# Optimization experiments

Hardware: AMD Instinct MI355X
Metric: run time of the kernel (lower is better)

Reference implementation:

```python
import jax, jax.numpy as jnp
import numpy as np

B, L, D, H = 2, 2048, 1024, 16


def setup_inputs() -> dict:
    key = jax.random.key(0)
    ks = jax.random.split(key, 6)
    return {
        "x": jax.random.normal(ks[0], (B, L, D), dtype=jnp.float32),
        "w_qkv": jax.random.normal(ks[1], (3 * D, D), dtype=jnp.float32) * (D ** -0.5),
        "b_qkv": jax.random.normal(ks[2], (3 * D,), dtype=jnp.float32) * 0.02,
        "w_out": jax.random.normal(ks[3], (D, D), dtype=jnp.float32) * (D ** -0.5),
        "b_out": jax.random.normal(ks[4], (D,), dtype=jnp.float32) * 0.02,
        "lam": jnp.float32(0.5),
        "heads": H,
    }


def reference(x, w_qkv, b_qkv, w_out, b_out, lam, heads):
    b, l, d = x.shape
    dh = d // heads
    scale = d ** -0.5  # NOTE: module scales by d_model**-0.5, not head_dim**-0.5

    qkv = x @ w_qkv.T + b_qkv                      # [B, L, 3D]
    qkv = qkv.reshape(b, l, 3, heads, dh)
    qkv = jnp.transpose(qkv, (2, 0, 3, 1, 4))      # [3, B, H, L, dh]
    q, k, v = qkv[0], qkv[1], qkv[2]

    k_prev = jnp.roll(k, shift=1, axis=2)          # roll along sequence dim

    s_cur = jnp.einsum("bhqd,bhkd->bhqk", q, k) * scale
    s_prev = jnp.einsum("bhqd,bhkd->bhqk", q, k_prev) * scale

    a1 = jax.nn.softmax(s_cur, axis=-1)
    a2 = jax.nn.softmax(s_prev, axis=-1)
    diff = lam * (a1 - a2)                         # dropout = identity (eval)

    o = jnp.einsum("bhqk,bhkd->bhqd", diff, v)     # [B, H, L, dh]
    o = jnp.transpose(o, (0, 2, 1, 3)).reshape(b, l, d)
    return o @ w_out.T + b_out
```

## Files before the change

### kernel.cpp

```cpp
#include <hip/hip_runtime.h>
#include <hip/hip_bf16.h>
#include <stdint.h>


typedef __attribute__((ext_vector_type(8))) short s16x8;
typedef __attribute__((ext_vector_type(4))) short s16x4;
typedef __attribute__((ext_vector_type(4))) float f32x4;

__device__ __forceinline__ float bf2f(unsigned short u) {
    union { unsigned int i; float f; } x; x.i = ((unsigned int)u) << 16; return x.f;
}
__device__ __forceinline__ unsigned short f2bf(float f) {
    union { float f; unsigned int i; } x; x.f = f;
    unsigned int r = x.i + 0x7FFFu + ((x.i >> 16) & 1u);
    return (unsigned short)(r >> 16);
}

__device__ __forceinline__ f32x4 mfma16(s16x4 a, s16x4 b, f32x4 c) {
#if __has_builtin(__builtin_amdgcn_mfma_f32_16x16x16bf16_1k)
    return __builtin_amdgcn_mfma_f32_16x16x16bf16_1k(a, b, c, 0, 0, 0);
#else
    f32x4 d;
    asm volatile("v_mfma_f32_16x16x16_bf16 %0, %1, %2, %3\n\ts_nop 7\n\ts_nop 3"
                 : "=v"(d) : "v"(a), "v"(b), "v"(c));
    return d;
#endif
}

__device__ __forceinline__ void gload16(const void* g, void* l) {
    auto gp = reinterpret_cast<const __attribute__((address_space(1))) unsigned int*>(
        reinterpret_cast<uintptr_t>(g));
    auto lp = reinterpret_cast<__attribute__((address_space(3))) unsigned int*>(
        reinterpret_cast<uintptr_t>(l));
    __builtin_amdgcn_global_load_lds(gp, lp, 16, 0, 0);
}

__global__ __launch_bounds__(256) void cvt_all(
    const float* __restrict__ x, const float* __restrict__ wq,
    const float* __restrict__ wo,
    unsigned short* __restrict__ xb, unsigned short* __restrict__ wqb,
    unsigned short* __restrict__ wob)
{
    int i4 = blockIdx.x * 256 + threadIdx.x;
    const float* src; unsigned short* dst; int off;
    if (i4 < 1048576)            { src = x;  dst = xb;  off = i4; }
    else if (i4 < 1048576 + 786432) { src = wq; dst = wqb; off = i4 - 1048576; }
    else                         { src = wo; dst = wob; off = i4 - 1835008; }
    float4 v = ((const float4*)src)[off];
    ushort4 u;
    u.x = f2bf(v.x); u.y = f2bf(v.y); u.z = f2bf(v.z); u.w = f2bf(v.w);
    ((ushort4*)dst)[off] = u;
}

__global__ __launch_bounds__(256) void vd_transpose(
    const unsigned short* __restrict__ qkvb, unsigned short* __restrict__ vdt)
{
    __shared__ unsigned short T[64][72];
    const int tid = threadIdx.x;
    const int j0 = blockIdx.x * 64;
    const int bh = blockIdx.y, b = bh >> 4, h = bh & 15;
    const unsigned short* vb = qkvb + (size_t)b * 2048 * 3072 + 2048 + h * 64;

    int r = tid >> 2, cq = tid & 3;
    int j = j0 + r, jn = (j + 1) & 2047;
    const unsigned short* p0 = vb + (size_t)j  * 3072 + cq * 16;
    const unsigned short* p1 = vb + (size_t)jn * 3072 + cq * 16;
    s16x8 a0 = *(const s16x8*)p0, a1 = *(const s16x8*)(p0 + 8);
    s16x8 b0 = *(const s16x8*)p1, b1 = *(const s16x8*)(p1 + 8);
#pragma unroll
    for (int u = 0; u < 8; ++u)
        T[cq * 16 + u][r] = f2bf(bf2f((unsigned short)a0[u]) - bf2f((unsigned short)b0[u]));
#pragma unroll
    for (int u = 0; u < 8; ++u)
        T[cq * 16 + 8 + u][r] = f2bf(bf2f((unsigned short)a1[u]) - bf2f((unsigned short)b1[u]));
    __syncthreads();

    int row = tid >> 2, sc = tid & 3;
    s16x8 o0 = *(const s16x8*)&T[row][sc * 16];
    s16x8 o1 = *(const s16x8*)&T[row][sc * 16 + 8];
    unsigned short* dst = vdt + ((size_t)bh * 64 + row) * 2048 + j0 + sc * 16;
    *(s16x8*)dst = o0;
    *(s16x8*)(dst + 8) = o1;
}

template <int OUT_BF16, int BN>
__global__ __launch_bounds__(256) void gemm_nt_mfma(
    const unsigned short* __restrict__ A,
    const unsigned short* __restrict__ Bm,
    const float* __restrict__ bias,
    void* __restrict__ C,
    int M, int N, int K, int nscale, float smul)
{
    constexpr int NT = BN / 32;
    __shared__ unsigned short As[2][128][32];
    __shared__ unsigned short Bs[2][BN][32];

    const int tid = threadIdx.x;
    const int wave = tid >> 6, lane = tid & 63;
    const int quad = lane >> 4, ln = lane & 15;
    const int wm = (wave >> 1) * 64, wn = (wave & 1) * (NT * 16);
    const int m0 = blockIdx.y * 128, n0 = blockIdx.x * BN;
    const int rA = wave * 16 + (lane >> 2);
    const int gsl = lane & 3;

    f32x4 acc[4][NT];
#pragma unroll
    for (int mt = 0; mt < 4; ++mt)
#pragma unroll
        for (int nt = 0; nt < NT; ++nt) acc[mt][nt] = f32x4{0.f, 0.f, 0.f, 0.f};

    auto stage = [&](int p, int k0) {
#pragma unroll
        for (int q = 0; q < 2; ++q) {
            int row = q * 64 + rA;
            int kg = gsl ^ ((row >> 1) & 3);
            gload16(A + (size_t)(m0 + row) * K + k0 + kg * 8,
                    &As[p][q * 64 + wave * 16][0]);
            if (q * 64 < BN)
                gload16(Bm + (size_t)(n0 + row) * K + k0 + kg * 8,
                        &Bs[p][q * 64 + wave * 16][0]);
        }
    };

    stage(0, 0);
    __syncthreads();
    int p = 0;
    for (int k0 = 0; k0 < K; k0 += 32) {
        if (k0 + 32 < K) stage(p ^ 1, k0 + 32);
        s16x8 af[4], bfr[NT];
#pragma unroll
        for (int mt = 0; mt < 4; ++mt) {
            int rr = wm + mt * 16 + ln;
            af[mt] = *(const s16x8*)&As[p][rr][((quad ^ ((rr >> 1) & 3)) & 3) * 8];
        }
#pragma unroll
        for (int nt = 0; nt < NT; ++nt) {
            int rr = wn + nt * 16 + ln;
            bfr[nt] = *(const s16x8*)&Bs[p][rr][((quad ^ ((rr >> 1) & 3)) & 3) * 8];
        }
#pragma unroll
        for (int mt = 0; mt < 4; ++mt)
#pragma unroll
            for (int nt = 0; nt < NT; ++nt)
                acc[mt][nt] = __builtin_amdgcn_mfma_f32_16x16x32_bf16(
                    af[mt], bfr[nt], acc[mt][nt], 0, 0, 0);
        __syncthreads();
        p ^= 1;
    }

    float bb[NT];
#pragma unroll
    for (int nt = 0; nt < NT; ++nt) bb[nt] = bias[n0 + wn + nt * 16 + ln];
#pragma unroll
    for (int mt = 0; mt < 4; ++mt)
#pragma unroll
        for (int nt = 0; nt < NT; ++nt) {
            int col = n0 + wn + nt * 16 + ln;
            float sc = (col < nscale) ? smul : 1.f;
#pragma unroll
            for (int rg = 0; rg < 4; ++rg) {
                int row = m0 + wm + mt * 16 + quad * 4 + rg;
                float v = (acc[mt][nt][rg] + bb[nt]) * sc;
                if (OUT_BF16)
                    ((unsigned short*)C)[(size_t)row * N + col] = f2bf(v);
                else
                    ((float*)C)[(size_t)row * N + col] = v;
            }
        }
}

__global__ __launch_bounds__(256) void diff_attn_v5(
    const unsigned short* __restrict__ qkv,
    const unsigned short* __restrict__ vdt,
    const float* __restrict__ lam_p,
    unsigned short* __restrict__ o_ws)
{
    constexpr int L = 2048, TD = 3072;

    __shared__ unsigned short Ks[2][64][64];
    __shared__ unsigned short Vs[2][64][64];

    const int tid = threadIdx.x;
    const int wave = tid >> 6, lane = tid & 63;
    const int quad = lane >> 4, ln = lane & 15;
    const int bh = blockIdx.y, b = bh >> 4, h = bh & 15;
    const int q0 = blockIdx.x * 128;
    const size_t seqbase = (size_t)b * L;
    const unsigned short* base = qkv + seqbase * TD + h * 64;
    const unsigned short* kb = base + 1024;
    const unsigned short* vbase = vdt + (size_t)bh * 64 * 2048;

    const int lsl = lane >> 3;
    const int cgl = (lane & 7) ^ lsl;

    s16x8 qf[2][2];
#pragma unroll
    for (int s = 0; s < 2; ++s) {
        const unsigned short* qrow =
            base + (size_t)(q0 + wave * 32 + s * 16 + ln) * TD;
        qf[s][0] = *(const s16x8*)(qrow + quad * 8);
        qf[s][1] = *(const s16x8*)(qrow + 32 + quad * 8);
    }

    auto stage = [&](int p, int j0) {
        const unsigned short* k0p = kb + (size_t)(j0 + wave * 16 + lsl) * TD + cgl * 8;
        gload16(k0p,                  &Ks[p][wave * 16][0]);
        gload16(k0p + (size_t)8 * TD, &Ks[p][wave * 16 + 8][0]);
        const unsigned short* v0p = vbase + (size_t)(wave * 16 + lsl) * 2048 + j0 + cgl * 8;
        gload16(v0p,            &Vs[p][wave * 16][0]);
        gload16(v0p + 8 * 2048, &Vs[p][wave * 16 + 8][0]);
    };

    f32x4 Ot[2][4];
    f32x4 lacc[2];
#pragma unroll
    for (int s = 0; s < 2; ++s) {
        lacc[s] = f32x4{0.f, 0.f, 0.f, 0.f};
#pragma unroll
        for (int mt = 0; mt < 4; ++mt) Ot[s][mt] = f32x4{0.f, 0.f, 0.f, 0.f};
    }

    const s16x4 ones = {(short)0x3F80, (short)0x3F80, (short)0x3F80, (short)0x3F80};
    const int kx0 = (quad ^ (ln & 7)) << 3;
    const int kx1 = ((quad + 4) ^ (ln & 7)) << 3;

    stage(0, 0);
    __syncthreads();
    int p = 0;
    for (int kt = 0; kt < 32; ++kt) {
        if (kt + 1 < 32) stage(p ^ 1, (kt + 1) * 64);

        f32x4 ST[2][4];
#pragma unroll
        for (int t = 0; t < 4; ++t) {
            s16x8 k0 = *(const s16x8*)&Ks[p][t * 16 + ln][kx0];
            s16x8 k1 = *(const s16x8*)&Ks[p][t * 16 + ln][kx1];
#pragma unroll
            for (int s = 0; s < 2; ++s) {
                f32x4 z = f32x4{0.f, 0.f, 0.f, 0.f};
                z = __builtin_amdgcn_mfma_f32_16x16x32_bf16(k0, qf[s][0], z, 0, 0, 0);
                z = __builtin_amdgcn_mfma_f32_16x16x32_bf16(k1, qf[s][1], z, 0, 0, 0);
                ST[s][t] = z;
            }
        }

        s16x4 pf[2][4];
#pragma unroll
        for (int s = 0; s < 2; ++s)
#pragma unroll
            for (int t = 0; t < 4; ++t) {
                unsigned int b0 = __builtin_bit_cast(unsigned int,
                    __builtin_amdgcn_exp2f(ST[s][t][0]));
                unsigned int b1 = __builtin_bit_cast(unsigned int,
                    __builtin_amdgcn_exp2f(ST[s][t][1]));
                unsigned int b2 = __builtin_bit_cast(unsigned int,
                    __builtin_amdgcn_exp2f(ST[s][t][2]));
                unsigned int b3 = __builtin_bit_cast(unsigned int,
                    __builtin_amdgcn_exp2f(ST[s][t][3]));
                unsigned int lo = (b0 >> 16) | (b1 & 0xFFFF0000u);
                unsigned int hi = (b2 >> 16) | (b3 & 0xFFFF0000u);
                uint2 pk = make_uint2(lo, hi);
                pf[s][t] = __builtin_bit_cast(s16x4, pk);
            }

#pragma unroll
        for (int s = 0; s < 2; ++s)
#pragma unroll
            for (int t = 0; t < 4; ++t)
                lacc[s] = mfma16(ones, pf[s][t], lacc[s]);

#pragma unroll
        for (int t = 0; t < 4; ++t) {
#pragma unroll
            for (int mt = 0; mt < 4; ++mt) {
                int chunk = (2 * t + (quad >> 1)) ^ (ln & 7);
                s16x4 vf = *(const s16x4*)&Vs[p][mt * 16 + ln][chunk * 8 + (quad & 1) * 4];
#pragma unroll
                for (int s = 0; s < 2; ++s)
                    Ot[s][mt] = mfma16(vf, pf[s][t], Ot[s][mt]);
            }
        }
        __syncthreads();
        p ^= 1;
    }

    const float lam = lam_p[0];
#pragma unroll
    for (int s = 0; s < 2; ++s) {
        float inv = lam / lacc[s][0];
        int row = q0 + wave * 32 + s * 16 + ln;
        unsigned short* orow = o_ws + (seqbase + row) * 1024 + h * 64 + quad * 4;
#pragma unroll
        for (int mt = 0; mt < 4; ++mt) {
            ushort4 u;
            u.x = f2bf(Ot[s][mt][0] * inv);
            u.y = f2bf(Ot[s][mt][1] * inv);
            u.z = f2bf(Ot[s][mt][2] * inv);
            u.w = f2bf(Ot[s][mt][3] * inv);
            *(ushort4*)(orow + mt * 16) = u;
        }
    }
}

extern "C" void kernel_launch(void* const* d_in, const int* in_sizes, int n_in,
                              void* d_out, int out_size, void* d_ws, size_t ws_size,
                              hipStream_t stream) {
    const float* x     = (const float*)d_in[0];
    const float* w_qkv = (const float*)d_in[1];
    const float* b_qkv = (const float*)d_in[2];
    const float* w_out = (const float*)d_in[3];
    const float* b_out = (const float*)d_in[4];
    const float* lam   = (const float*)d_in[5];
    float* out = (float*)d_out;

    unsigned short* xb   = (unsigned short*)d_ws;
    unsigned short* wqb  = xb   + (size_t)4096 * 1024;
    unsigned short* wob  = wqb  + (size_t)3072 * 1024;
    unsigned short* qkvb = wob  + (size_t)1024 * 1024;
    unsigned short* ob   = qkvb + (size_t)4096 * 3072;
    unsigned short* vdt  = ob   + (size_t)4096 * 1024;

    cvt_all<<<8192, 256, 0, stream>>>(x, w_qkv, w_out, xb, wqb, wob);

    gemm_nt_mfma<1, 128><<<dim3(24, 32), 256, 0, stream>>>(
        xb, wqb, b_qkv, qkvb, 4096, 3072, 1024, 1024, 0.045084222f);

    vd_transpose<<<dim3(32, 32), 256, 0, stream>>>(qkvb, vdt);

    diff_attn_v5<<<dim3(16, 32), 256, 0, stream>>>(qkvb, vdt, lam, ob);

    gemm_nt_mfma<0, 64><<<dim3(16, 32), 256, 0, stream>>>(
        ob, wob, b_out, out, 4096, 1024, 1024, 0, 1.f);
}
```

Measured before the change: 198.4 us.

## Use 16x16x32 MFMA for PV via permlane swaps and halve query tile

The attention kernel now converts exp'd scores into operands for the 16x16x32 bf16 MFMA using v_permlane32/16_swap, replacing the 16x16x16 MFMAs for both the row-sum and PV products. It also reads V with 8-element vector loads matching the K swizzle. Each block now handles 64 query rows instead of 128, one 16-row slice per wave, and the grid doubles. Fewer, wider MFMAs and more blocks should raise throughput and occupancy, but K/V tiles are reused across half as many queries per block, doubling their global and LDS traffic.

```diff
diff --git a/kernel.cpp b/kernel.cpp
--- a/kernel.cpp
+++ b/kernel.cpp
@@ -4,7 +4,6 @@
 
 
 typedef __attribute__((ext_vector_type(8))) short s16x8;
-typedef __attribute__((ext_vector_type(4))) short s16x4;
 typedef __attribute__((ext_vector_type(4))) float f32x4;
 
 __device__ __forceinline__ float bf2f(unsigned short u) {
@@ -14,17 +13,6 @@
     union { float f; unsigned int i; } x; x.f = f;
     unsigned int r = x.i + 0x7FFFu + ((x.i >> 16) & 1u);
     return (unsigned short)(r >> 16);
-}
-
-__device__ __forceinline__ f32x4 mfma16(s16x4 a, s16x4 b, f32x4 c) {
-#if __has_builtin(__builtin_amdgcn_mfma_f32_16x16x16bf16_1k)
-    return __builtin_amdgcn_mfma_f32_16x16x16bf16_1k(a, b, c, 0, 0, 0);
-#else
-    f32x4 d;
-    asm volatile("v_mfma_f32_16x16x16_bf16 %0, %1, %2, %3\n\ts_nop 7\n\ts_nop 3"
-                 : "=v"(d) : "v"(a), "v"(b), "v"(c));
-    return d;
-#endif
 }
 
 __device__ __forceinline__ void gload16(const void* g, void* l) {
@@ -169,7 +157,7 @@
         }
 }
 
-__global__ __launch_bounds__(256) void diff_attn_v5(
+__global__ __launch_bounds__(256) void diff_attn_v6(
     const unsigned short* __restrict__ qkv,
     const unsigned short* __restrict__ vdt,
     const float* __restrict__ lam_p,
@@ -184,7 +172,7 @@
     const int wave = tid >> 6, lane = tid & 63;
     const int quad = lane >> 4, ln = lane & 15;
     const int bh = blockIdx.y, b = bh >> 4, h = bh & 15;
-    const int q0 = blockIdx.x * 128;
+    const int q0 = blockIdx.x * 64;
     const size_t seqbase = (size_t)b * L;
     const unsigned short* base = qkv + seqbase * TD + h * 64;
     const unsigned short* kb = base + 1024;
@@ -193,13 +181,11 @@
     const int lsl = lane >> 3;
     const int cgl = (lane & 7) ^ lsl;
 
-    s16x8 qf[2][2];
-#pragma unroll
-    for (int s = 0; s < 2; ++s) {
-        const unsigned short* qrow =
-            base + (size_t)(q0 + wave * 32 + s * 16 + ln) * TD;
-        qf[s][0] = *(const s16x8*)(qrow + quad * 8);
-        qf[s][1] = *(const s16x8*)(qrow + 32 + quad * 8);
+    s16x8 qf0, qf1;
+    {
+        const unsigned short* qrow = base + (size_t)(q0 + wave * 16 + ln) * TD;
+        qf0 = *(const s16x8*)(qrow + quad * 8);
+        qf1 = *(const s16x8*)(qrow + 32 + quad * 8);
     }
 
     auto stage = [&](int p, int j0) {
@@ -211,16 +197,14 @@
         gload16(v0p + 8 * 2048, &Vs[p][wave * 16 + 8][0]);
     };
 
-    f32x4 Ot[2][4];
-    f32x4 lacc[2];
-#pragma unroll
-    for (int s = 0; s < 2; ++s) {
-        lacc[s] = f32x4{0.f, 0.f, 0.f, 0.f};
-#pragma unroll
-        for (int mt = 0; mt < 4; ++mt) Ot[s][mt] = f32x4{0.f, 0.f, 0.f, 0.f};
-    }
-
-    const s16x4 ones = {(short)0x3F80, (short)0x3F80, (short)0x3F80, (short)0x3F80};
+    f32x4 Ot[4];
+    f32x4 lacc;
+    lacc = f32x4{0.f, 0.f, 0.f, 0.f};
+#pragma unroll
+    for (int mt = 0; mt < 4; ++mt) Ot[mt] = f32x4{0.f, 0.f, 0.f, 0.f};
+
+    const s16x8 ones8 = {(short)0x3F80, (short)0x3F80, (short)0x3F80, (short)0x3F80,
+                         (short)0x3F80, (short)0x3F80, (short)0x3F80, (short)0x3F80};
     const int kx0 = (quad ^ (ln & 7)) << 3;
     const int kx1 = ((quad + 4) ^ (ln & 7)) << 3;
 
@@ -230,54 +214,51 @@
     for (int kt = 0; kt < 32; ++kt) {
         if (kt + 1 < 32) stage(p ^ 1, (kt + 1) * 64);
 
-        f32x4 ST[2][4];
+        f32x4 ST[4];
 #pragma unroll
         for (int t = 0; t < 4; ++t) {
             s16x8 k0 = *(const s16x8*)&Ks[p][t * 16 + ln][kx0];
             s16x8 k1 = *(const s16x8*)&Ks[p][t * 16 + ln][kx1];
-#pragma unroll
-            for (int s = 0; s < 2; ++s) {
-                f32x4 z = f32x4{0.f, 0.f, 0.f, 0.f};
-                z = __builtin_amdgcn_mfma_f32_16x16x32_bf16(k0, qf[s][0], z, 0, 0, 0);
-                z = __builtin_amdgcn_mfma_f32_16x16x32_bf16(k1, qf[s][1], z, 0, 0, 0);
-                ST[s][t] = z;
-            }
-        }
-
-        s16x4 pf[2][4];
-#pragma unroll
-        for (int s = 0; s < 2; ++s)
-#pragma unroll
-            for (int t = 0; t < 4; ++t) {
-                unsigned int b0 = __builtin_bit_cast(unsigned int,
-                    __builtin_amdgcn_exp2f(ST[s][t][0]));
-                unsigned int b1 = __builtin_bit_cast(unsigned int,
-                    __builtin_amdgcn_exp2f(ST[s][t][1]));
-                unsigned int b2 = __builtin_bit_cast(unsigned int,
-                    __builtin_amdgcn_exp2f(ST[s][t][2]));
-                unsigned int b3 = __builtin_bit_cast(unsigned int,
-                    __builtin_amdgcn_exp2f(ST[s][t][3]));
-                unsigned int lo = (b0 >> 16) | (b1 & 0xFFFF0000u);
-                unsigned int hi = (b2 >> 16) | (b3 & 0xFFFF0000u);
-                uint2 pk = make_uint2(lo, hi);
-                pf[s][t] = __builtin_bit_cast(s16x4, pk);
-            }
-
-#pragma unroll
-        for (int s = 0; s < 2; ++s)
-#pragma unroll
-            for (int t = 0; t < 4; ++t)
-                lacc[s] = mfma16(ones, pf[s][t], lacc[s]);
-
+            f32x4 z = f32x4{0.f, 0.f, 0.f, 0.f};
+            z = __builtin_amdgcn_mfma_f32_16x16x32_bf16(k0, qf0, z, 0, 0, 0);
+            z = __builtin_amdgcn_mfma_f32_16x16x32_bf16(k1, qf1, z, 0, 0, 0);
+            ST[t] = z;
+        }
+
+        uint2 pk[4];
 #pragma unroll
         for (int t = 0; t < 4; ++t) {
+            unsigned int e0 = __builtin_bit_cast(unsigned int, __builtin_amdgcn_exp2f(ST[t][0]));
+            unsigned int e1 = __builtin_bit_cast(unsigned int, __builtin_amdgcn_exp2f(ST[t][1]));
+            unsigned int e2 = __builtin_bit_cast(unsigned int, __builtin_amdgcn_exp2f(ST[t][2]));
+            unsigned int e3 = __builtin_bit_cast(unsigned int, __builtin_amdgcn_exp2f(ST[t][3]));
+            pk[t].x = (e0 >> 16) | (e1 & 0xFFFF0000u);
+            pk[t].y = (e2 >> 16) | (e3 & 0xFFFF0000u);
+        }
+
+        s16x8 pfr[2];
+#pragma unroll
+        for (int bb = 0; bb < 2; ++bb) {
+            unsigned int a0 = pk[2 * bb].x, b0 = pk[2 * bb + 1].x;
+            unsigned int a1 = pk[2 * bb].y, b1 = pk[2 * bb + 1].y;
+            asm volatile("v_permlane32_swap_b32 %0, %1" : "+v"(a0), "+v"(b0));
+            asm volatile("v_permlane16_swap_b32 %0, %1" : "+v"(a0), "+v"(b0));
+            asm volatile("v_permlane32_swap_b32 %0, %1" : "+v"(a1), "+v"(b1));
+            asm volatile("v_permlane16_swap_b32 %0, %1" : "+v"(a1), "+v"(b1));
+            uint4 fr = make_uint4(a0, a1, b0, b1);
+            pfr[bb] = __builtin_bit_cast(s16x8, fr);
+        }
+
+        lacc = __builtin_amdgcn_mfma_f32_16x16x32_bf16(ones8, pfr[0], lacc, 0, 0, 0);
+        lacc = __builtin_amdgcn_mfma_f32_16x16x32_bf16(ones8, pfr[1], lacc, 0, 0, 0);
+
+#pragma unroll
+        for (int bb = 0; bb < 2; ++bb) {
+            const int kx = bb ? kx1 : kx0;
 #pragma unroll
             for (int mt = 0; mt < 4; ++mt) {
-                int chunk = (2 * t + (quad >> 1)) ^ (ln & 7);
-                s16x4 vf = *(const s16x4*)&Vs[p][mt * 16 + ln][chunk * 8 + (quad & 1) * 4];
-#pragma unroll
-                for (int s = 0; s < 2; ++s)
-                    Ot[s][mt] = mfma16(vf, pf[s][t], Ot[s][mt]);
+                s16x8 vf = *(const s16x8*)&Vs[p][mt * 16 + ln][kx];
+                Ot[mt] = __builtin_amdgcn_mfma_f32_16x16x32_bf16(vf, pfr[bb], Ot[mt], 0, 0, 0);
             }
         }
         __syncthreads();
@@ -285,18 +266,17 @@
     }
 
     const float lam = lam_p[0];
-#pragma unroll
-    for (int s = 0; s < 2; ++s) {
-        float inv = lam / lacc[s][0];
-        int row = q0 + wave * 32 + s * 16 + ln;
+    {
+        float inv = lam / lacc[0];
+        int row = q0 + wave * 16 + ln;
         unsigned short* orow = o_ws + (seqbase + row) * 1024 + h * 64 + quad * 4;
 #pragma unroll
         for (int mt = 0; mt < 4; ++mt) {
             ushort4 u;
-            u.x = f2bf(Ot[s][mt][0] * inv);
-            u.y = f2bf(Ot[s][mt][1] * inv);
-            u.z = f2bf(Ot[s][mt][2] * inv);
-            u.w = f2bf(Ot[s][mt][3] * inv);
+            u.x = f2bf(Ot[mt][0] * inv);
+            u.y = f2bf(Ot[mt][1] * inv);
+            u.z = f2bf(Ot[mt][2] * inv);
+            u.w = f2bf(Ot[mt][3] * inv);
             *(ushort4*)(orow + mt * 16) = u;
         }
     }
@@ -327,7 +307,7 @@
 
     vd_transpose<<<dim3(32, 32), 256, 0, stream>>>(qkvb, vdt);
 
-    diff_attn_v5<<<dim3(16, 32), 256, 0, stream>>>(qkvb, vdt, lam, ob);
+    diff_attn_v6<<<dim3(32, 32), 256, 0, stream>>>(qkvb, vdt, lam, ob);
 
     gemm_nt_mfma<0, 64><<<dim3(16, 32), 256, 0, stream>>>(
         ob, wob, b_out, out, 4096, 1024, 1024, 0, 1.f);
```

Measured after the change: 199.7 us. No clear change (+0.7%).

## Use 16x16x32 MFMA for PV via permlane swaps; shrink attention blocks to two waves

Applied to the files above, without the earlier changes.

The PV product and row-sum accumulation move from 16x16x16 bf16 MFMAs to 16x16x32 MFMAs. The exp'd probability fragments are rearranged across lanes with v_permlane32/16_swap so they match the wider K-operand layout, and V is read as 8-element chunks reusing the K swizzle offsets. This halves the MFMA instruction count for that stage. The attention kernel also drops to 128 threads covering 64 query rows per block, doubling the grid, with each wave now staging 32 K/V rows. The cost is extra cross-lane swap instructions and fewer waves per block to hide load latency.

```diff
diff --git a/kernel.cpp b/kernel.cpp
--- a/kernel.cpp
+++ b/kernel.cpp
@@ -4,7 +4,6 @@
 
 
 typedef __attribute__((ext_vector_type(8))) short s16x8;
-typedef __attribute__((ext_vector_type(4))) short s16x4;
 typedef __attribute__((ext_vector_type(4))) float f32x4;
 
 __device__ __forceinline__ float bf2f(unsigned short u) {
@@ -14,17 +13,6 @@
     union { float f; unsigned int i; } x; x.f = f;
     unsigned int r = x.i + 0x7FFFu + ((x.i >> 16) & 1u);
     return (unsigned short)(r >> 16);
-}
-
-__device__ __forceinline__ f32x4 mfma16(s16x4 a, s16x4 b, f32x4 c) {
-#if __has_builtin(__builtin_amdgcn_mfma_f32_16x16x16bf16_1k)
-    return __builtin_amdgcn_mfma_f32_16x16x16bf16_1k(a, b, c, 0, 0, 0);
-#else
-    f32x4 d;
-    asm volatile("v_mfma_f32_16x16x16_bf16 %0, %1, %2, %3\n\ts_nop 7\n\ts_nop 3"
-                 : "=v"(d) : "v"(a), "v"(b), "v"(c));
-    return d;
-#endif
 }
 
 __device__ __forceinline__ void gload16(const void* g, void* l) {
@@ -169,7 +157,7 @@
         }
 }
 
-__global__ __launch_bounds__(256) void diff_attn_v5(
+__global__ __launch_bounds__(128) void diff_attn_v7(
     const unsigned short* __restrict__ qkv,
     const unsigned short* __restrict__ vdt,
     const float* __restrict__ lam_p,
@@ -184,7 +172,7 @@
     const int wave = tid >> 6, lane = tid & 63;
     const int quad = lane >> 4, ln = lane & 15;
     const int bh = blockIdx.y, b = bh >> 4, h = bh & 15;
-    const int q0 = blockIdx.x * 128;
+    const int q0 = blockIdx.x * 64;
     const size_t seqbase = (size_t)b * L;
     const unsigned short* base = qkv + seqbase * TD + h * 64;
     const unsigned short* kb = base + 1024;
@@ -203,12 +191,15 @@
     }
 
     auto stage = [&](int p, int j0) {
-        const unsigned short* k0p = kb + (size_t)(j0 + wave * 16 + lsl) * TD + cgl * 8;
-        gload16(k0p,                  &Ks[p][wave * 16][0]);
-        gload16(k0p + (size_t)8 * TD, &Ks[p][wave * 16 + 8][0]);
-        const unsigned short* v0p = vbase + (size_t)(wave * 16 + lsl) * 2048 + j0 + cgl * 8;
-        gload16(v0p,            &Vs[p][wave * 16][0]);
-        gload16(v0p + 8 * 2048, &Vs[p][wave * 16 + 8][0]);
+        const unsigned short* k0p = kb + (size_t)(j0 + wave * 32 + lsl) * TD + cgl * 8;
+#pragma unroll
+        for (int rr = 0; rr < 4; ++rr)
+            gload16(k0p + (size_t)(8 * rr) * TD, &Ks[p][wave * 32 + 8 * rr][0]);
+        const unsigned short* v0p =
+            vbase + (size_t)(wave * 32 + lsl) * 2048 + j0 + cgl * 8;
+#pragma unroll
+        for (int rr = 0; rr < 4; ++rr)
+            gload16(v0p + 8 * rr * 2048, &Vs[p][wave * 32 + 8 * rr][0]);
     };
 
     f32x4 Ot[2][4];
@@ -220,7 +211,8 @@
         for (int mt = 0; mt < 4; ++mt) Ot[s][mt] = f32x4{0.f, 0.f, 0.f, 0.f};
     }
 
-    const s16x4 ones = {(short)0x3F80, (short)0x3F80, (short)0x3F80, (short)0x3F80};
+    const s16x8 ones8 = {(short)0x3F80, (short)0x3F80, (short)0x3F80, (short)0x3F80,
+                         (short)0x3F80, (short)0x3F80, (short)0x3F80, (short)0x3F80};
     const int kx0 = (quad ^ (ln & 7)) << 3;
     const int kx1 = ((quad + 4) ^ (ln & 7)) << 3;
 
@@ -244,40 +236,44 @@
             }
         }
 
-        s16x4 pf[2][4];
-#pragma unroll
-        for (int s = 0; s < 2; ++s)
+        s16x8 pfr[2][2];
+#pragma unroll
+        for (int s = 0; s < 2; ++s) {
+            uint2 pk[4];
 #pragma unroll
             for (int t = 0; t < 4; ++t) {
-                unsigned int b0 = __builtin_bit_cast(unsigned int,
-                    __builtin_amdgcn_exp2f(ST[s][t][0]));
-                unsigned int b1 = __builtin_bit_cast(unsigned int,
-                    __builtin_amdgcn_exp2f(ST[s][t][1]));
-                unsigned int b2 = __builtin_bit_cast(unsigned int,
-                    __builtin_amdgcn_exp2f(ST[s][t][2]));
-                unsigned int b3 = __builtin_bit_cast(unsigned int,
-                    __builtin_amdgcn_exp2f(ST[s][t][3]));
-                unsigned int lo = (b0 >> 16) | (b1 & 0xFFFF0000u);
-                unsigned int hi = (b2 >> 16) | (b3 & 0xFFFF0000u);
-                uint2 pk = make_uint2(lo, hi);
-                pf[s][t] = __builtin_bit_cast(s16x4, pk);
-            }
-
-#pragma unroll
-        for (int s = 0; s < 2; ++s)
-#pragma unroll
-            for (int t = 0; t < 4; ++t)
-                lacc[s] = mfma16(ones, pf[s][t], lacc[s]);
-
-#pragma unroll
-        for (int t = 0; t < 4; ++t) {
+                unsigned int e0 = __builtin_bit_cast(unsigned int, __builtin_amdgcn_exp2f(ST[s][t][0]));
+                unsigned int e1 = __builtin_bit_cast(unsigned int, __builtin_amdgcn_exp2f(ST[s][t][1]));
+                unsigned int e2 = __builtin_bit_cast(unsigned int, __builtin_amdgcn_exp2f(ST[s][t][2]));
+                unsigned int e3 = __builtin_bit_cast(unsigned int, __builtin_amdgcn_exp2f(ST[s][t][3]));
+                pk[t].x = (e0 >> 16) | (e1 & 0xFFFF0000u);
+                pk[t].y = (e2 >> 16) | (e3 & 0xFFFF0000u);
+            }
+#pragma unroll
+            for (int bb = 0; bb < 2; ++bb) {
+                unsigned int a0 = pk[2 * bb].x, b0 = pk[2 * bb + 1].x;
+                unsigned int a1 = pk[2 * bb].y, b1 = pk[2 * bb + 1].y;
+                asm volatile("v_permlane32_swap_b32 %0, %1" : "+v"(a0), "+v"(b0));
+                asm volatile("v_permlane16_swap_b32 %0, %1" : "+v"(a0), "+v"(b0));
+                asm volatile("v_permlane32_swap_b32 %0, %1" : "+v"(a1), "+v"(b1));
+                asm volatile("v_permlane16_swap_b32 %0, %1" : "+v"(a1), "+v"(b1));
+                uint4 fr = make_uint4(a0, a1, b0, b1);
+                pfr[s][bb] = __builtin_bit_cast(s16x8, fr);
+            }
+            lacc[s] = __builtin_amdgcn_mfma_f32_16x16x32_bf16(ones8, pfr[s][0], lacc[s], 0, 0, 0);
+            lacc[s] = __builtin_amdgcn_mfma_f32_16x16x32_bf16(ones8, pfr[s][1], lacc[s], 0, 0, 0);
+        }
+
+#pragma unroll
+        for (int bb = 0; bb < 2; ++bb) {
+            const int kx = bb ? kx1 : kx0;
 #pragma unroll
             for (int mt = 0; mt < 4; ++mt) {
-                int chunk = (2 * t + (quad >> 1)) ^ (ln & 7);
-                s16x4 vf = *(const s16x4*)&Vs[p][mt * 16 + ln][chunk * 8 + (quad & 1) * 4];
+                s16x8 vf = *(const s16x8*)&Vs[p][mt * 16 + ln][kx];
 #pragma unroll
                 for (int s = 0; s < 2; ++s)
-                    Ot[s][mt] = mfma16(vf, pf[s][t], Ot[s][mt]);
+                    Ot[s][mt] = __builtin_amdgcn_mfma_f32_16x16x32_bf16(
+                        vf, pfr[s][bb], Ot[s][mt], 0, 0, 0);
             }
         }
         __syncthreads();
@@ -327,7 +323,7 @@
 
     vd_transpose<<<dim3(32, 32), 256, 0, stream>>>(qkvb, vdt);
 
-    diff_attn_v5<<<dim3(16, 32), 256, 0, stream>>>(qkvb, vdt, lam, ob);
+    diff_attn_v7<<<dim3(32, 32), 128, 0, stream>>>(qkvb, vdt, lam, ob);
 
     gemm_nt_mfma<0, 64><<<dim3(16, 32), 256, 0, stream>>>(
         ob, wob, b_out, out, 4096, 1024, 1024, 0, 1.f);
```

Measured after the change: 210.3 us. 1.06x slower.
